# Performance work log

Measured on AMD Instinct MI355X. Metric: run time of the kernel, lower is better.

The kernel has to match this reference:

```python
import jax, jax.numpy as jnp
import numpy as np

B, A, G = 8, 200000, 64
K = 4                       # max_k: top-k anchors per GT
T_LOW, T_HIGH = 0.3, 0.7    # matcher thresholds
NUM_SAMPLES, POS_FRAC = 256, 0.5  # batch_size_per_image, positive_fraction
MAX_POS = int(NUM_SAMPLES * POS_FRAC)  # 128


def cxcywh_to_xyxy(b):
    cx, cy, w, h = b[..., 0], b[..., 1], b[..., 2], b[..., 3]
    return jnp.stack([cx - 0.5 * w, cy - 0.5 * h, cx + 0.5 * w, cy + 0.5 * h], axis=-1)


def box_iou(b1, b2):
    # b1: [G,4], b2: [A,4] in xyxy -> iou [G,A]
    area1 = (b1[:, 2] - b1[:, 0]) * (b1[:, 3] - b1[:, 1])
    area2 = (b2[:, 2] - b2[:, 0]) * (b2[:, 3] - b2[:, 1])
    lt = jnp.maximum(b1[:, None, :2], b2[None, :, :2])
    rb = jnp.minimum(b1[:, None, 2:], b2[None, :, 2:])
    wh = jnp.clip(rb - lt, 0.0)
    inter = wh[..., 0] * wh[..., 1]
    union = area1[:, None] + area2[None, :] - inter
    return inter / union


def _per_image(anchors, gt, key):
    iou = box_iou(cxcywh_to_xyxy(gt), cxcywh_to_xyxy(anchors))  # [G, A]
    # --- Matcher(thresholds=[t_low, t_high], labels=[0,-1,1], allow_low_quality_matches=True)
    matched_vals = iou.max(axis=0)        # best IoU per anchor
    matches = jnp.argmax(iou, axis=0)     # matched GT per anchor
    labels = jnp.where(matched_vals >= T_HIGH, 1,
             jnp.where(matched_vals >= T_LOW, -1, 0))
    hq = iou.max(axis=1)                  # highest quality per GT
    labels = jnp.where((iou == hq[:, None]).any(axis=0), 1, labels)  # low-quality matches -> positive
    # --- subsample_labels: randomly keep at most 128 positives (negatives don't affect outputs)
    is_pos = labels == 1
    r = jax.random.uniform(key, (anchors.shape[0],))
    rank = jnp.argsort(jnp.argsort(jnp.where(is_pos, r, 2.0)))  # random rank among positives
    num_pos = jnp.minimum(MAX_POS, is_pos.sum())
    sel_pos = is_pos & (rank < num_pos)
    # --- sample_topk_per_gt: per GT keep min(count, K) top-IoU anchors (fixed-shape, padded with -1)
    counts = jax.ops.segment_sum(sel_pos.astype(jnp.int32), matches, num_segments=G)
    top_vals, top_idx = jax.lax.top_k(iou, K)  # [G, K]
    valid = jnp.arange(K)[None, :] < jnp.minimum(counts, K)[:, None]
    pr = jnp.where(valid, top_idx, -1).reshape(-1)
    gt_i = jnp.where(valid, jnp.arange(G)[:, None], -1).reshape(-1)
    scores = jnp.where(valid, top_vals, 0.0).reshape(-1)
    return pr, gt_i, valid.reshape(-1), scores


def setup_inputs() -> dict:
    key = jax.random.key(0)
    k1, k2 = jax.random.split(key)
    anchors = jax.random.uniform(k1, (B, A, 4), dtype=jnp.float32)   # cxcywh
    gt_boxes = jax.random.uniform(k2, (B, G, 4), dtype=jnp.float32)  # cxcywh
    return {"anchors": anchors, "gt_boxes": gt_boxes}


def reference(anchors, gt_boxes):
    # Returns padded (pr_inds, gt_inds, valid_mask, topk_ious), each [B, G*K];
    # invalid slots hold -1 indices (padding for the variable-length torch output).
    keys = jax.random.split(jax.random.key(42), anchors.shape[0])
    return jax.vmap(_per_image)(anchors, gt_boxes, keys)
```

## Files before the change

kernel.cpp:

```cpp
#include <hip/hip_runtime.h>
#include <stdint.h>


#pragma clang fp contract(off)

#define B_IMG 8
#define A_N 200000
#define G_N 64
#define K_TOP 4
#define MAX_POS 128
#define FINE_CAP 4096
#define AS 2048
#define NS 98
#define SUB_NS 8
#define WPS 32
#define NWORD 3136

typedef unsigned long long u64;
typedef unsigned int u32;

__device__ __forceinline__ u32 rotl32(u32 v, int n) { return (v << n) | (v >> (32 - n)); }

__device__ __forceinline__ void tf_round(u32& x0, u32& x1, int r) {
  x0 += x1; x1 = rotl32(x1, r); x1 ^= x0;
}

__device__ __forceinline__ void threefry2x32(u32 k0, u32 k1, u32& x0, u32& x1) {
  u32 ks2 = 0x1BD11BDAu ^ k0 ^ k1;
  x0 += k0; x1 += k1;
  tf_round(x0,x1,13); tf_round(x0,x1,15); tf_round(x0,x1,26); tf_round(x0,x1,6);
  x0 += k1; x1 += ks2 + 1u;
  tf_round(x0,x1,17); tf_round(x0,x1,29); tf_round(x0,x1,16); tf_round(x0,x1,24);
  x0 += ks2; x1 += k0 + 2u;
  tf_round(x0,x1,13); tf_round(x0,x1,15); tf_round(x0,x1,26); tf_round(x0,x1,6);
  x0 += k0; x1 += k1 + 3u;
  tf_round(x0,x1,17); tf_round(x0,x1,29); tf_round(x0,x1,16); tf_round(x0,x1,24);
  x0 += k1; x1 += ks2 + 4u;
  tf_round(x0,x1,13); tf_round(x0,x1,15); tf_round(x0,x1,26); tf_round(x0,x1,6);
  x0 += ks2; x1 += k0 + 5u;
}

__device__ __forceinline__ void image_key(int b, u32& kb0, u32& kb1) {
  u32 x0 = 0u, x1 = (u32)b;
  threefry2x32(0u, 42u, x0, x1);
  kb0 = x0; kb1 = x1;
}

__device__ __forceinline__ u32 rbits_for(u32 k0, u32 k1, u32 a) {
  u32 x0 = 0u, x1 = a;
  threefry2x32(k0, k1, x0, x1);
  return x0 ^ x1;
}

__device__ __forceinline__ void conv_box(float4 bx, float& x0, float& y0,
                                         float& x1, float& y1, float& area) {
  #pragma clang fp contract(off)
  x0 = bx.x - 0.5f * bx.z;
  y0 = bx.y - 0.5f * bx.w;
  x1 = bx.x + 0.5f * bx.z;
  y1 = bx.y + 0.5f * bx.w;
  area = (x1 - x0) * (y1 - y0);
}

__device__ __forceinline__ float iou_pair(float ax0, float ay0, float ax1, float ay1, float aarea,
                                          float gx0, float gy0, float gx1, float gy1, float garea) {
  #pragma clang fp contract(off)
  float ltx = fmaxf(gx0, ax0), lty = fmaxf(gy0, ay0);
  float rbx = fminf(gx1, ax1), rby = fminf(gy1, ay1);
  float w = fmaxf(rbx - ltx, 0.0f), h = fmaxf(rby - lty, 0.0f);
  float inter = w * h;
  float uni = (garea + aarea) - inter;
  return inter / uni;
}

__device__ __forceinline__ void iou_parts(float ax0, float ay0, float ax1, float ay1, float aarea,
                                          float gx0, float gy0, float gx1, float gy1, float garea,
                                          float& inter, float& uni) {
  #pragma clang fp contract(off)
  float ltx = fmaxf(gx0, ax0), lty = fmaxf(gy0, ay0);
  float rbx = fminf(gx1, ax1), rby = fminf(gy1, ay1);
  float w = fmaxf(rbx - ltx, 0.0f), h = fmaxf(rby - lty, 0.0f);
  inter = w * h;
  uni = (garea + aarea) - inter;
}

__device__ __forceinline__ void top4_insert(u64 (&top)[4], u64 key) {
  if (key > top[3]) {
    if (key > top[0])      { top[3]=top[2]; top[2]=top[1]; top[1]=top[0]; top[0]=key; }
    else if (key > top[1]) { top[3]=top[2]; top[2]=top[1]; top[1]=key; }
    else if (key > top[2]) { top[3]=top[2]; top[2]=key; }
    else                   { top[3]=key; }
  }
}

__device__ __forceinline__ void wave_merge_top4(u64 (&top)[4]) {
  for (int off = 32; off >= 1; off >>= 1) {
    u64 o[4];
    #pragma unroll
    for (int k = 0; k < 4; k++) o[k] = __shfl_down(top[k], (unsigned)off);
    u64 m[4]; int i = 0, j = 0;
    #pragma unroll
    for (int k = 0; k < 4; k++) m[k] = (top[i] >= o[j]) ? top[i++] : o[j++];
    #pragma unroll
    for (int k = 0; k < 4; k++) top[k] = m[k];
  }
}

__device__ __forceinline__ void wave_merge_top4_u32(u32 (&top)[4]) {
  for (int off = 32; off >= 1; off >>= 1) {
    u32 o[4];
    #pragma unroll
    for (int k = 0; k < 4; k++) o[k] = __shfl_down(top[k], (unsigned)off);
    u32 m[4]; int i = 0, j = 0;
    #pragma unroll
    for (int k = 0; k < 4; k++) m[k] = (top[i] >= o[j]) ? top[i++] : o[j++];
    #pragma unroll
    for (int k = 0; k < 4; k++) top[k] = m[k];
  }
}

__device__ __forceinline__ float screen_thresh(u32 tau) {
  u32 tb = (tau > 8u) ? (tau - 8u) : 0u;
  return __uint_as_float(tb);
}

__launch_bounds__(512, 4)
__global__ void k_thresh(const float4* __restrict__ anchors, const float4* __restrict__ gt,
                         u32* __restrict__ thr_part,
                         u32* __restrict__ npos, u32* __restrict__ fcnt,
                         u32* __restrict__ cnt) {
  const int s = blockIdx.x;
  const int b = blockIdx.y;
  const int t = threadIdx.x;
  const int wave = t >> 6, lane = t & 63;

  __shared__ float4 sxy[AS];
  __shared__ float  sg[5][64];

  if (s == 0) {
    if (t < 64) cnt[b * G_N + t] = 0;
    if (t == 0) { fcnt[b] = 0; npos[b] = 0; }
  }

  const int base = s * AS;
  const float4* ab = anchors + (size_t)b * A_N + base;

  for (int j = t; j < AS; j += 512) {
    float x0, y0, x1, y1, ar;
    conv_box(ab[j], x0, y0, x1, y1, ar);
    sxy[j] = make_float4(x0, y0, x1, y1);
  }
  if (t < 64) {
    float x0, y0, x1, y1, ar;
    conv_box(gt[(size_t)b * G_N + t], x0, y0, x1, y1, ar);
    sg[0][t] = x0; sg[1][t] = y0; sg[2][t] = x1; sg[3][t] = y1; sg[4][t] = ar;
  }
  __syncthreads();

  for (int gg = 0; gg < 2; gg++) {
    const int gi = (wave * 2 + gg) * 4;
    const float g0x0 = sg[0][gi],   g0y0 = sg[1][gi],   g0x1 = sg[2][gi],   g0y1 = sg[3][gi],   g0a = sg[4][gi];
    const float g1x0 = sg[0][gi+1], g1y0 = sg[1][gi+1], g1x1 = sg[2][gi+1], g1y1 = sg[3][gi+1], g1a = sg[4][gi+1];
    const float g2x0 = sg[0][gi+2], g2y0 = sg[1][gi+2], g2x1 = sg[2][gi+2], g2y1 = sg[3][gi+2], g2a = sg[4][gi+2];
    const float g3x0 = sg[0][gi+3], g3y0 = sg[1][gi+3], g3x1 = sg[2][gi+3], g3y1 = sg[3][gi+3], g3a = sg[4][gi+3];

    u32 q0 = 0, q1 = 0, q2 = 0, q3 = 0;
    for (int j = lane; j < AS; j += 64) {
      float4 x = sxy[j];
      float aarea = (x.z - x.x) * (x.w - x.y);
      float i0, u0, i1, u1, i2, u2, i3, u3;
      iou_parts(x.x, x.y, x.z, x.w, aarea, g0x0, g0y0, g0x1, g0y1, g0a, i0, u0);
      iou_parts(x.x, x.y, x.z, x.w, aarea, g1x0, g1y0, g1x1, g1y1, g1a, i1, u1);
      iou_parts(x.x, x.y, x.z, x.w, aarea, g2x0, g2y0, g2x1, g2y1, g2a, i2, u2);
      iou_parts(x.x, x.y, x.z, x.w, aarea, g3x0, g3y0, g3x1, g3y1, g3a, i3, u3);
      q0 = max(q0, __float_as_uint(i0 * __builtin_amdgcn_rcpf(u0)));
      q1 = max(q1, __float_as_uint(i1 * __builtin_amdgcn_rcpf(u1)));
      q2 = max(q2, __float_as_uint(i2 * __builtin_amdgcn_rcpf(u2)));
      q3 = max(q3, __float_as_uint(i3 * __builtin_amdgcn_rcpf(u3)));
    }
    u32 Q0[4] = {q0,0,0,0}, Q1[4] = {q1,0,0,0}, Q2[4] = {q2,0,0,0}, Q3[4] = {q3,0,0,0};
    wave_merge_top4_u32(Q0);
    wave_merge_top4_u32(Q1);
    wave_merge_top4_u32(Q2);
    wave_merge_top4_u32(Q3);
    if (lane == 0) {
      u32* dst = thr_part + ((size_t)b * SUB_NS + s) * G_N + gi;
      dst[0] = Q0[3]; dst[1] = Q1[3]; dst[2] = Q2[3]; dst[3] = Q3[3];
    }
  }
}

__launch_bounds__(512, 4)
__global__ void k_main(const float4* __restrict__ anchors, const float4* __restrict__ gt,
                       const u32* __restrict__ thr_part,
                       u64* __restrict__ partial,
                       u64* __restrict__ posA, u64* __restrict__ posB) {
  const int s = blockIdx.x;
  const int b = blockIdx.y;
  const int t = threadIdx.x;
  const int wave = t >> 6, lane = t & 63;

  __shared__ float4 sxy[AS];
  __shared__ float  sg[5][64];
  __shared__ float  sthr[64];
  u32* wm = (u32*)sxy;

  const int base = s * AS;
  const int acnt = min(AS, A_N - base);
  const float4* ab = anchors + (size_t)b * A_N + base;

  for (int j = t; j < acnt; j += 512) {
    float x0, y0, x1, y1, ar;
    conv_box(ab[j], x0, y0, x1, y1, ar);
    sxy[j] = make_float4(x0, y0, x1, y1);
  }
  if (t < 64) {
    float x0, y0, x1, y1, ar;
    conv_box(gt[(size_t)b * G_N + t], x0, y0, x1, y1, ar);
    sg[0][t] = x0; sg[1][t] = y0; sg[2][t] = x1; sg[3][t] = y1; sg[4][t] = ar;
    u32 mx = 0;
    for (int ss = 0; ss < SUB_NS; ss++)
      mx = max(mx, thr_part[((size_t)b * SUB_NS + ss) * G_N + t]);
    const u32 L7 = 0x3F333333u - 8u;
    sthr[t] = screen_thresh(min(mx > 16u ? mx - 16u : 0u, L7));
  }
  __syncthreads();

  u32 m = 0;
  for (int gg = 0; gg < 2; gg++) {
    const int gp = wave * 2 + gg;
    const int gi = gp * 4;
    const float g0x0 = sg[0][gi],   g0y0 = sg[1][gi],   g0x1 = sg[2][gi],   g0y1 = sg[3][gi],   g0a = sg[4][gi];
    const float g1x0 = sg[0][gi+1], g1y0 = sg[1][gi+1], g1x1 = sg[2][gi+1], g1y1 = sg[3][gi+1], g1a = sg[4][gi+1];
    const float g2x0 = sg[0][gi+2], g2y0 = sg[1][gi+2], g2x1 = sg[2][gi+2], g2y1 = sg[3][gi+2], g2a = sg[4][gi+2];
    const float g3x0 = sg[0][gi+3], g3y0 = sg[1][gi+3], g3x1 = sg[2][gi+3], g3y1 = sg[3][gi+3], g3a = sg[4][gi+3];
    const float t0 = sthr[gi], t1 = sthr[gi+1], t2 = sthr[gi+2], t3 = sthr[gi+3];

    u64 T0[4] = {0,0,0,0}, T1[4] = {0,0,0,0}, T2[4] = {0,0,0,0}, T3[4] = {0,0,0,0};
    u32 h0 = 0, h1 = 0, h2 = 0, h3 = 0;
    u32 bit = 1u;
    for (int j = lane; j < acnt; j += 64, bit <<= 1) {
      float4 x = sxy[j];
      float aarea = (x.z - x.x) * (x.w - x.y);
      float i0, u0, i1, u1, i2, u2, i3, u3;
      iou_parts(x.x, x.y, x.z, x.w, aarea, g0x0, g0y0, g0x1, g0y1, g0a, i0, u0);
      iou_parts(x.x, x.y, x.z, x.w, aarea, g1x0, g1y0, g1x1, g1y1, g1a, i1, u1);
      iou_parts(x.x, x.y, x.z, x.w, aarea, g2x0, g2y0, g2x1, g2y1, g2a, i2, u2);
      iou_parts(x.x, x.y, x.z, x.w, aarea, g3x0, g3y0, g3x1, g3y1, g3a, i3, u3);
      u32 ni = ~(u32)(base + j);
      bool s0 = (i0 >= t0 * u0), s1 = (i1 >= t1 * u1);
      bool s2 = (i2 >= t2 * u2), s3 = (i3 >= t3 * u3);
      if (__ballot(s0)) {
        float v = 0.0f;
        if (s0) { v = i0 / u0; if (v >= 0.7f) m |= bit; }
        u32 vb = __float_as_uint(v);
        bool ins = s0 && (vb >= h0);
        if (__ballot(ins)) {
          if (ins) top4_insert(T0, ((u64)vb << 32) | (u64)ni);
          h0 = (u32)(T0[3] >> 32);
        }
      }
      if (__ballot(s1)) {
        float v = 0.0f;
        if (s1) { v = i1 / u1; if (v >= 0.7f) m |= bit; }
        u32 vb = __float_as_uint(v);
        bool ins = s1 && (vb >= h1);
        if (__ballot(ins)) {
          if (ins) top4_insert(T1, ((u64)vb << 32) | (u64)ni);
          h1 = (u32)(T1[3] >> 32);
        }
      }
      if (__ballot(s2)) {
        float v = 0.0f;
        if (s2) { v = i2 / u2; if (v >= 0.7f) m |= bit; }
        u32 vb = __float_as_uint(v);
        bool ins = s2 && (vb >= h2);
        if (__ballot(ins)) {
          if (ins) top4_insert(T2, ((u64)vb << 32) | (u64)ni);
          h2 = (u32)(T2[3] >> 32);
        }
      }
      if (__ballot(s3)) {
        float v = 0.0f;
        if (s3) { v = i3 / u3; if (v >= 0.7f) m |= bit; }
        u32 vb = __float_as_uint(v);
        bool ins = s3 && (vb >= h3);
        if (__ballot(ins)) {
          if (ins) top4_insert(T3, ((u64)vb << 32) | (u64)ni);
          h3 = (u32)(T3[3] >> 32);
        }
      }
    }
    wave_merge_top4(T0);
    wave_merge_top4(T1);
    wave_merge_top4(T2);
    wave_merge_top4(T3);
    if (lane == 0) {
      u64* dst = partial + (((size_t)b * NS + s) * G_N + gi) * 4;
      #pragma unroll
      for (int k = 0; k < 4; k++) {
        dst[k] = T0[k]; dst[4 + k] = T1[k]; dst[8 + k] = T2[k]; dst[12 + k] = T3[k];
      }
    }
  }

  __syncthreads();
  wm[t] = m;
  __syncthreads();
  if (wave == 0 || wave == 4) {
    const u32* wmh = wm + (wave & 4) * 64;
    u32 mc = wmh[lane] | wmh[64 + lane] | wmh[128 + lane] | wmh[192 + lane];
    u64* posH = (wave ? posB : posA) + (size_t)b * NWORD + s * WPS;
    for (int k = 0; k < WPS; k++) {
      u64 bal = __ballot((mc >> k) & 1u);
      if (lane == 0) posH[k] = bal;
    }
  }
}

__launch_bounds__(64)
__global__ void k_top4_merge(const u64* __restrict__ partial, u64* __restrict__ top4,
                             u64* __restrict__ posA) {
  const int b = blockIdx.y, g = blockIdx.x, lane = threadIdx.x;
  const u64* pb = partial + ((size_t)b * NS * G_N + g) * 4;
  u64 keys[7];
  int nk = 0;
  for (int i = lane; i < NS * 4; i += 64)
    keys[nk++] = pb[(size_t)(i >> 2) * (G_N * 4) + (i & 3)];
  u64 top[4] = {0ull, 0ull, 0ull, 0ull};
  for (int q = 0; q < nk; q++) top4_insert(top, keys[q]);
  wave_merge_top4(top);
  if (lane == 0) {
    u64* dst = top4 + ((size_t)b * G_N + g) * 4;
    #pragma unroll
    for (int k = 0; k < 4; k++) dst[k] = top[k];
  }
  u32 hqb = (u32)(__shfl(top[0], 0) >> 32);
  for (int q = 0; q < nk; q++) {
    u64 key = keys[q];
    u32 aidx = ~(u32)key;
    if ((u32)(key >> 32) == hqb && aidx < A_N)
      atomicOr(&posA[(size_t)b * NWORD + (aidx >> 6)], 1ull << (aidx & 63));
  }
}

__launch_bounds__(256)
__global__ void k_zero(u32* __restrict__ hist) {
  int i = blockIdx.x * 256 + threadIdx.x;
  if (i < B_IMG * 4096) hist[i] = 0;
}

__launch_bounds__(256)
__global__ void k_hist(const u64* __restrict__ posA, const u64* __restrict__ posB,
                       u32* __restrict__ npos, u32* __restrict__ hist) {
  const int b = blockIdx.y;
  const int i = blockIdx.x * 256 + threadIdx.x;
  u32 k0, k1; image_key(b, k0, k1);
  u32 c = 0;
  if (i < NWORD) {
    u64 w = posA[(size_t)b * NWORD + i] | posB[(size_t)b * NWORD + i];
    c = (u32)__popcll(w);
    while (w) {
      int bit = __ffsll((long long)w) - 1; w &= w - 1;
      u32 a = (u32)(i * 64 + bit);
      atomicAdd(&hist[b * 4096 + (rbits_for(k0, k1, a) >> 20)], 1u);
    }
  }
  #pragma unroll
  for (int off = 32; off >= 1; off >>= 1) c += __shfl_xor(c, off);
  if ((threadIdx.x & 63) == 0 && c) atomicAdd(&npos[b], c);
}

__launch_bounds__(256)
__global__ void k_collect(const u64* __restrict__ posA, const u64* __restrict__ posB,
                          const u32* __restrict__ npos, const u32* __restrict__ hist,
                          int2* __restrict__ binsel,
                          u32* __restrict__ fine, u32* __restrict__ fcnt) {
  const int b = blockIdx.y;
  const int t = threadIdx.x;
  __shared__ u32 red[256];
  __shared__ int sbin;

  const u32* hb = hist + b * 4096;
  u32 local = 0;
  for (int j = 0; j < 16; j++) local += hb[t * 16 + j];
  red[t] = local;
  __syncthreads();
  if (t == 0) {
    if (npos[b] <= MAX_POS) {
      sbin = -1;
      binsel[b] = make_int2(-1, 0);
    } else {
      u32 cum = 0; int chunk = 0;
      for (int i = 0; i < 256; i++) {
        if (cum + red[i] >= MAX_POS) { chunk = i; break; }
        cum += red[i];
      }
      int tb = chunk * 16; u32 before = cum;
      for (int j = 0; j < 16; j++) {
        u32 h = hb[chunk * 16 + j];
        if (before + h >= MAX_POS) { tb = chunk * 16 + j; break; }
        before += h;
      }
      sbin = tb;
      binsel[b] = make_int2(tb, (int)before);
    }
  }
  __syncthreads();
  const int stb = sbin;
  if (stb < 0) return;

  u32 k0, k1; image_key(b, k0, k1);
  const int a0 = blockIdx.x * AS;
  const u64* pa = posA + (size_t)b * NWORD;
  const u64* pb = posB + (size_t)b * NWORD;
  for (int j = t; j < AS; j += 256) {
    int a = a0 + j;
    if (a >= A_N) break;
    if (!(((pa[a >> 6] | pb[a >> 6]) >> (a & 63)) & 1ull)) continue;
    u32 rb = rbits_for(k0, k1, (u32)a);
    if ((int)(rb >> 20) != stb) continue;
    u32 idx = atomicAdd(&fcnt[b], 1u);
    if (idx < FINE_CAP) fine[b * FINE_CAP + idx] = (((rb >> 9) & 0x7FFu) << 18) | (u32)a;
  }
}

__launch_bounds__(256)
__global__ void k_count(const float4* __restrict__ anchors, const float4* __restrict__ gt,
                        const u64* __restrict__ posA, const u64* __restrict__ posB,
                        const int2* __restrict__ binsel, const u32* __restrict__ fine,
                        const u32* __restrict__ fcnt, u32* __restrict__ cnt) {
  const int b = blockIdx.y;
  const int t = threadIdx.x;
  __shared__ float sg[5][64];
  __shared__ u64 sT;

  if (t < 64) {
    float x0, y0, x1, y1, ar;
    conv_box(gt[(size_t)b * G_N + t], x0, y0, x1, y1, ar);
    sg[0][t] = x0; sg[1][t] = y0; sg[2][t] = x1; sg[3][t] = y1; sg[4][t] = ar;
    int2 bs = binsel[b];
    u64 T = ~0ull;
    if (bs.x >= 0) {
      const int m = min((int)fcnt[b], FINE_CAP);
      const u32 need = (u32)(MAX_POS - bs.y);
      const u32* fb = fine + b * FINE_CAP;
      u32 lo = 0, hi = (1u << 29) - 1;
      while (lo < hi) {
        u32 mid = lo + ((hi - lo) >> 1);
        u32 c = 0;
        for (int j = t; j < m; j += 64) c += (fb[j] <= mid) ? 1u : 0u;
        #pragma unroll
        for (int off = 32; off >= 1; off >>= 1) c += __shfl_xor(c, off);
        if (c >= need) hi = mid; else lo = mid + 1;
      }
      T = ((u64)(u32)bs.x << 29) | (u64)lo;
    }
    if (t == 0) sT = T;
  }
  __syncthreads();

  u32 k0, k1; image_key(b, k0, k1);
  const u64 T = sT;
  const int a0 = blockIdx.x * AS;
  const u64* pa = posA + (size_t)b * NWORD;
  const u64* pb = posB + (size_t)b * NWORD;
  const float4* ab = anchors + (size_t)b * A_N;
  for (int j = t; j < AS; j += 256) {
    int a = a0 + j;
    if (a >= A_N) break;
    if (!(((pa[a >> 6] | pb[a >> 6]) >> (a & 63)) & 1ull)) continue;
    if (T != ~0ull) {
      u32 rb = rbits_for(k0, k1, (u32)a);
      if (((((u64)(rb >> 9)) << 18) | (u64)(u32)a) > T) continue;
    }
    float ax0, ay0, ax1, ay1, aar;
    conv_box(ab[a], ax0, ay0, ax1, ay1, aar);
    float bv = -1.0f; int g0 = 0;
    for (int g = 0; g < 64; g++) {
      float v = iou_pair(ax0, ay0, ax1, ay1, aar,
                         sg[0][g], sg[1][g], sg[2][g], sg[3][g], sg[4][g]);
      if (v > bv) { bv = v; g0 = g; }
    }
    atomicAdd(&cnt[b * G_N + g0], 1u);
  }
}

__launch_bounds__(64)
__global__ void k_out(const u64* __restrict__ top4, const u32* __restrict__ cnt,
                      float* __restrict__ out, int sec) {
  const int b = blockIdx.x;
  const int g = threadIdx.x;
  const u32 c = min(cnt[b * G_N + g], (u32)K_TOP);
  const u64* t4 = top4 + ((size_t)b * G_N + g) * 4;
  #pragma unroll
  for (int k = 0; k < 4; k++) {
    u64 key = t4[k];
    u32 fb = (u32)(key >> 32);
    u32 aidx = ~(u32)key;
    bool valid = (u32)k < c;
    int o = b * (G_N * K_TOP) + g * K_TOP + k;
    out[0 * sec + o] = valid ? (float)aidx : -1.0f;
    out[1 * sec + o] = valid ? (float)g : -1.0f;
    out[2 * sec + o] = valid ? 1.0f : 0.0f;
    out[3 * sec + o] = valid ? __uint_as_float(fb) : 0.0f;
  }
}

extern "C" void kernel_launch(void* const* d_in, const int* in_sizes, int n_in,
                              void* d_out, int out_size, void* d_ws, size_t ws_size,
                              hipStream_t stream) {
  const float4* anchors = (const float4*)d_in[0];
  const float4* gt      = (const float4*)d_in[1];
  float* out = (float*)d_out;

  char* ws = (char*)d_ws;
  u64*  top4    = (u64*)(ws);
  u32*  thr_prt = (u32*)(ws);
  u64*  partial = (u64*)(ws + 16384);
  u32*  fine    = (u32*)(ws + 16384);
  u32*  hist    = (u32*)(ws + 147456);
  int2* binsel  = (int2*)(ws + 278528);
  u64*  posA    = (u64*)(ws + 1622016);
  u64*  posB    = (u64*)(ws + 1822720);
  u32*  npos    = (u32*)(ws + 2023424);
  u32*  fcnt    = (u32*)(ws + 2023456);
  u32*  cnt     = (u32*)(ws + 2023488);

  int sec = out_size / 4;

  k_thresh    <<<dim3(SUB_NS, B_IMG), 512, 0, stream>>>(anchors, gt, thr_prt, npos, fcnt, cnt);
  k_main      <<<dim3(NS, B_IMG), 512, 0, stream>>>(anchors, gt, thr_prt, partial, posA, posB);
  k_top4_merge<<<dim3(G_N, B_IMG), 64, 0, stream>>>(partial, top4, posA);
  k_zero      <<<dim3(128), 256, 0, stream>>>(hist);
  k_hist      <<<dim3(13, B_IMG), 256, 0, stream>>>(posA, posB, npos, hist);
  k_collect   <<<dim3(NS, B_IMG), 256, 0, stream>>>(posA, posB, npos, hist, binsel, fine, fcnt);
  k_count     <<<dim3(NS, B_IMG), 256, 0, stream>>>(anchors, gt, posA, posB, binsel, fine, fcnt, cnt);
  k_out       <<<dim3(B_IMG), 64, 0, stream>>>(top4, cnt, out, sec);
}
```

Baseline: 271.4 us.

## Fuse histogram building into main and merge kernels, drop posB and two launches

The positive-anchor histogram and count are now built inside k_main, from the merged wave masks, and in k_top4_merge for low-quality matches that newly set a bit. The separate zero and hist kernels are removed, histogram zeroing moves into k_thresh, and the posB bitmap is folded into a single posA. A combined ballot also skips per-GT branch checks when no lane passes the screen. This saves two launches and a pass over the bitmaps, at the cost of more global atomics in k_main and k_top4_merge.

```diff
diff --git a/kernel.cpp b/kernel.cpp
--- a/kernel.cpp
+++ b/kernel.cpp
@@ -126,7 +126,7 @@
 
 __launch_bounds__(512, 4)
 __global__ void k_thresh(const float4* __restrict__ anchors, const float4* __restrict__ gt,
-                         u32* __restrict__ thr_part,
+                         u32* __restrict__ thr_part, u32* __restrict__ hist,
                          u32* __restrict__ npos, u32* __restrict__ fcnt,
                          u32* __restrict__ cnt) {
   const int s = blockIdx.x;
@@ -137,6 +137,7 @@
   __shared__ float4 sxy[AS];
   __shared__ float  sg[5][64];
 
+  hist[(b * SUB_NS + s) * 512 + t] = 0;
   if (s == 0) {
     if (t < 64) cnt[b * G_N + t] = 0;
     if (t == 0) { fcnt[b] = 0; npos[b] = 0; }
@@ -193,8 +194,8 @@
 __launch_bounds__(512, 4)
 __global__ void k_main(const float4* __restrict__ anchors, const float4* __restrict__ gt,
                        const u32* __restrict__ thr_part,
-                       u64* __restrict__ partial,
-                       u64* __restrict__ posA, u64* __restrict__ posB) {
+                       u64* __restrict__ partial, u64* __restrict__ posA,
+                       u32* __restrict__ hist, u32* __restrict__ npos) {
   const int s = blockIdx.x;
   const int b = blockIdx.y;
   const int t = threadIdx.x;
@@ -247,47 +248,49 @@
       iou_parts(x.x, x.y, x.z, x.w, aarea, g1x0, g1y0, g1x1, g1y1, g1a, i1, u1);
       iou_parts(x.x, x.y, x.z, x.w, aarea, g2x0, g2y0, g2x1, g2y1, g2a, i2, u2);
       iou_parts(x.x, x.y, x.z, x.w, aarea, g3x0, g3y0, g3x1, g3y1, g3a, i3, u3);
-      u32 ni = ~(u32)(base + j);
       bool s0 = (i0 >= t0 * u0), s1 = (i1 >= t1 * u1);
       bool s2 = (i2 >= t2 * u2), s3 = (i3 >= t3 * u3);
-      if (__ballot(s0)) {
-        float v = 0.0f;
-        if (s0) { v = i0 / u0; if (v >= 0.7f) m |= bit; }
-        u32 vb = __float_as_uint(v);
-        bool ins = s0 && (vb >= h0);
-        if (__ballot(ins)) {
-          if (ins) top4_insert(T0, ((u64)vb << 32) | (u64)ni);
-          h0 = (u32)(T0[3] >> 32);
+      if (__ballot(s0 || s1 || s2 || s3)) {
+        u32 ni = ~(u32)(base + j);
+        if (__ballot(s0)) {
+          float v = 0.0f;
+          if (s0) { v = i0 / u0; if (v >= 0.7f) m |= bit; }
+          u32 vb = __float_as_uint(v);
+          bool ins = s0 && (vb >= h0);
+          if (__ballot(ins)) {
+            if (ins) top4_insert(T0, ((u64)vb << 32) | (u64)ni);
+            h0 = (u32)(T0[3] >> 32);
+          }
         }
-      }
-      if (__ballot(s1)) {
-        float v = 0.0f;
-        if (s1) { v = i1 / u1; if (v >= 0.7f) m |= bit; }
-        u32 vb = __float_as_uint(v);
-        bool ins = s1 && (vb >= h1);
-        if (__ballot(ins)) {
-          if (ins) top4_insert(T1, ((u64)vb << 32) | (u64)ni);
-          h1 = (u32)(T1[3] >> 32);
+        if (__ballot(s1)) {
+          float v = 0.0f;
+          if (s1) { v = i1 / u1; if (v >= 0.7f) m |= bit; }
+          u32 vb = __float_as_uint(v);
+          bool ins = s1 && (vb >= h1);
+          if (__ballot(ins)) {
+            if (ins) top4_insert(T1, ((u64)vb << 32) | (u64)ni);
+            h1 = (u32)(T1[3] >> 32);
+          }
         }
-      }
-      if (__ballot(s2)) {
-        float v = 0.0f;
-        if (s2) { v = i2 / u2; if (v >= 0.7f) m |= bit; }
-        u32 vb = __float_as_uint(v);
-        bool ins = s2 && (vb >= h2);
-        if (__ballot(ins)) {
-          if (ins) top4_insert(T2, ((u64)vb << 32) | (u64)ni);
-          h2 = (u32)(T2[3] >> 32);
+        if (__ballot(s2)) {
+          float v = 0.0f;
+          if (s2) { v = i2 / u2; if (v >= 0.7f) m |= bit; }
+          u32 vb = __float_as_uint(v);
+          bool ins = s2 && (vb >= h2);
+          if (__ballot(ins)) {
+            if (ins) top4_insert(T2, ((u64)vb << 32) | (u64)ni);
+            h2 = (u32)(T2[3] >> 32);
+          }
         }
-      }
-      if (__ballot(s3)) {
-        float v = 0.0f;
-        if (s3) { v = i3 / u3; if (v >= 0.7f) m |= bit; }
-        u32 vb = __float_as_uint(v);
-        bool ins = s3 && (vb >= h3);
-        if (__ballot(ins)) {
-          if (ins) top4_insert(T3, ((u64)vb << 32) | (u64)ni);
-          h3 = (u32)(T3[3] >> 32);
+        if (__ballot(s3)) {
+          float v = 0.0f;
+          if (s3) { v = i3 / u3; if (v >= 0.7f) m |= bit; }
+          u32 vb = __float_as_uint(v);
+          bool ins = s3 && (vb >= h3);
+          if (__ballot(ins)) {
+            if (ins) top4_insert(T3, ((u64)vb << 32) | (u64)ni);
+            h3 = (u32)(T3[3] >> 32);
+          }
         }
       }
     }
@@ -307,20 +310,33 @@
   __syncthreads();
   wm[t] = m;
   __syncthreads();
-  if (wave == 0 || wave == 4) {
-    const u32* wmh = wm + (wave & 4) * 64;
-    u32 mc = wmh[lane] | wmh[64 + lane] | wmh[128 + lane] | wmh[192 + lane];
-    u64* posH = (wave ? posB : posA) + (size_t)b * NWORD + s * WPS;
+  if (wave == 0) {
+    u32 mc = 0;
+    #pragma unroll
+    for (int w = 0; w < 8; w++) mc |= wm[w * 64 + lane];
+    u64* posH = posA + (size_t)b * NWORD + s * WPS;
     for (int k = 0; k < WPS; k++) {
       u64 bal = __ballot((mc >> k) & 1u);
       if (lane == 0) posH[k] = bal;
     }
+    u32 k0, k1; image_key(b, k0, k1);
+    u32 c = (u32)__popc(mc);
+    u32 mm = mc;
+    while (mm) {
+      int k = __ffs((int)mm) - 1; mm &= mm - 1;
+      u32 a = (u32)(base + k * 64 + lane);
+      atomicAdd(&hist[b * 4096 + (rbits_for(k0, k1, a) >> 20)], 1u);
+    }
+    #pragma unroll
+    for (int off = 32; off >= 1; off >>= 1) c += __shfl_xor(c, off);
+    if (lane == 0 && c) atomicAdd(&npos[b], c);
   }
 }
 
 __launch_bounds__(64)
 __global__ void k_top4_merge(const u64* __restrict__ partial, u64* __restrict__ top4,
-                             u64* __restrict__ posA) {
+                             u64* __restrict__ posA,
+                             u32* __restrict__ hist, u32* __restrict__ npos) {
   const int b = blockIdx.y, g = blockIdx.x, lane = threadIdx.x;
   const u64* pb = partial + ((size_t)b * NS * G_N + g) * 4;
   u64 keys[7];
@@ -336,43 +352,23 @@
     for (int k = 0; k < 4; k++) dst[k] = top[k];
   }
   u32 hqb = (u32)(__shfl(top[0], 0) >> 32);
+  u32 kk0, kk1; image_key(b, kk0, kk1);
   for (int q = 0; q < nk; q++) {
     u64 key = keys[q];
     u32 aidx = ~(u32)key;
-    if ((u32)(key >> 32) == hqb && aidx < A_N)
-      atomicOr(&posA[(size_t)b * NWORD + (aidx >> 6)], 1ull << (aidx & 63));
+    if ((u32)(key >> 32) == hqb && aidx < A_N) {
+      u64 bit = 1ull << (aidx & 63);
+      u64 old = atomicOr(&posA[(size_t)b * NWORD + (aidx >> 6)], bit);
+      if (!(old & bit)) {
+        atomicAdd(&hist[b * 4096 + (rbits_for(kk0, kk1, aidx) >> 20)], 1u);
+        atomicAdd(&npos[b], 1u);
+      }
+    }
   }
 }
 
 __launch_bounds__(256)
-__global__ void k_zero(u32* __restrict__ hist) {
-  int i = blockIdx.x * 256 + threadIdx.x;
-  if (i < B_IMG * 4096) hist[i] = 0;
-}
-
-__launch_bounds__(256)
-__global__ void k_hist(const u64* __restrict__ posA, const u64* __restrict__ posB,
-                       u32* __restrict__ npos, u32* __restrict__ hist) {
-  const int b = blockIdx.y;
-  const int i = blockIdx.x * 256 + threadIdx.x;
-  u32 k0, k1; image_key(b, k0, k1);
-  u32 c = 0;
-  if (i < NWORD) {
-    u64 w = posA[(size_t)b * NWORD + i] | posB[(size_t)b * NWORD + i];
-    c = (u32)__popcll(w);
-    while (w) {
-      int bit = __ffsll((long long)w) - 1; w &= w - 1;
-      u32 a = (u32)(i * 64 + bit);
-      atomicAdd(&hist[b * 4096 + (rbits_for(k0, k1, a) >> 20)], 1u);
-    }
-  }
-  #pragma unroll
-  for (int off = 32; off >= 1; off >>= 1) c += __shfl_xor(c, off);
-  if ((threadIdx.x & 63) == 0 && c) atomicAdd(&npos[b], c);
-}
-
-__launch_bounds__(256)
-__global__ void k_collect(const u64* __restrict__ posA, const u64* __restrict__ posB,
+__global__ void k_collect(const u64* __restrict__ posA,
                           const u32* __restrict__ npos, const u32* __restrict__ hist,
                           int2* __restrict__ binsel,
                           u32* __restrict__ fine, u32* __restrict__ fcnt) {
@@ -413,11 +409,10 @@
   u32 k0, k1; image_key(b, k0, k1);
   const int a0 = blockIdx.x * AS;
   const u64* pa = posA + (size_t)b * NWORD;
-  const u64* pb = posB + (size_t)b * NWORD;
   for (int j = t; j < AS; j += 256) {
     int a = a0 + j;
     if (a >= A_N) break;
-    if (!(((pa[a >> 6] | pb[a >> 6]) >> (a & 63)) & 1ull)) continue;
+    if (!((pa[a >> 6] >> (a & 63)) & 1ull)) continue;
     u32 rb = rbits_for(k0, k1, (u32)a);
     if ((int)(rb >> 20) != stb) continue;
     u32 idx = atomicAdd(&fcnt[b], 1u);
@@ -427,7 +422,7 @@
 
 __launch_bounds__(256)
 __global__ void k_count(const float4* __restrict__ anchors, const float4* __restrict__ gt,
-                        const u64* __restrict__ posA, const u64* __restrict__ posB,
+                        const u64* __restrict__ posA,
                         const int2* __restrict__ binsel, const u32* __restrict__ fine,
                         const u32* __restrict__ fcnt, u32* __restrict__ cnt) {
   const int b = blockIdx.y;
@@ -464,12 +459,11 @@
   const u64 T = sT;
   const int a0 = blockIdx.x * AS;
   const u64* pa = posA + (size_t)b * NWORD;
-  const u64* pb = posB + (size_t)b * NWORD;
   const float4* ab = anchors + (size_t)b * A_N;
   for (int j = t; j < AS; j += 256) {
     int a = a0 + j;
     if (a >= A_N) break;
-    if (!(((pa[a >> 6] | pb[a >> 6]) >> (a & 63)) & 1ull)) continue;
+    if (!((pa[a >> 6] >> (a & 63)) & 1ull)) continue;
     if (T != ~0ull) {
       u32 rb = rbits_for(k0, k1, (u32)a);
       if (((((u64)(rb >> 9)) << 18) | (u64)(u32)a) > T) continue;
@@ -519,22 +513,19 @@
   u32*  thr_prt = (u32*)(ws);
   u64*  partial = (u64*)(ws + 16384);
   u32*  fine    = (u32*)(ws + 16384);
-  u32*  hist    = (u32*)(ws + 147456);
-  int2* binsel  = (int2*)(ws + 278528);
+  int2* binsel  = (int2*)(ws + 147456);
   u64*  posA    = (u64*)(ws + 1622016);
-  u64*  posB    = (u64*)(ws + 1822720);
-  u32*  npos    = (u32*)(ws + 2023424);
-  u32*  fcnt    = (u32*)(ws + 2023456);
-  u32*  cnt     = (u32*)(ws + 2023488);
+  u32*  hist    = (u32*)(ws + 1822720);
+  u32*  npos    = (u32*)(ws + 1953792);
+  u32*  fcnt    = (u32*)(ws + 1953824);
+  u32*  cnt     = (u32*)(ws + 1953856);
 
   int sec = out_size / 4;
 
-  k_thresh    <<<dim3(SUB_NS, B_IMG), 512, 0, stream>>>(anchors, gt, thr_prt, npos, fcnt, cnt);
-  k_main      <<<dim3(NS, B_IMG), 512, 0, stream>>>(anchors, gt, thr_prt, partial, posA, posB);
-  k_top4_merge<<<dim3(G_N, B_IMG), 64, 0, stream>>>(partial, top4, posA);
-  k_zero      <<<dim3(128), 256, 0, stream>>>(hist);
-  k_hist      <<<dim3(13, B_IMG), 256, 0, stream>>>(posA, posB, npos, hist);
-  k_collect   <<<dim3(NS, B_IMG), 256, 0, stream>>>(posA, posB, npos, hist, binsel, fine, fcnt);
-  k_count     <<<dim3(NS, B_IMG), 256, 0, stream>>>(anchors, gt, posA, posB, binsel, fine, fcnt, cnt);
+  k_thresh    <<<dim3(SUB_NS, B_IMG), 512, 0, stream>>>(anchors, gt, thr_prt, hist, npos, fcnt, cnt);
+  k_main      <<<dim3(NS, B_IMG), 512, 0, stream>>>(anchors, gt, thr_prt, partial, posA, hist, npos);
+  k_top4_merge<<<dim3(G_N, B_IMG), 64, 0, stream>>>(partial, top4, posA, hist, npos);
+  k_collect   <<<dim3(NS, B_IMG), 256, 0, stream>>>(posA, npos, hist, binsel, fine, fcnt);
+  k_count     <<<dim3(NS, B_IMG), 256, 0, stream>>>(anchors, gt, posA, binsel, fine, fcnt, cnt);
   k_out       <<<dim3(B_IMG), 64, 0, stream>>>(top4, cnt, out, sec);
 }
```

Result: no change. 270.6 us (-0.3%).
